# Optimization experiments

Measured on AMD Instinct MI355X. Metric: run time of the kernel, lower is better.

## Reference

```python
import jax, jax.numpy as jnp
import numpy as np

N_NODES = 100000


def gcn_conv(x, edge_index, W, b, n_nodes):
    """PyG GCNConv: linear -> add self-loops -> symmetric-normalized scatter-sum -> bias."""
    h = x @ W  # [N, F_out]
    loop = jnp.arange(n_nodes, dtype=edge_index.dtype)
    src = jnp.concatenate([edge_index[0], loop])
    dst = jnp.concatenate([edge_index[1], loop])
    # degree of destination nodes (self-loops included)
    deg = jax.ops.segment_sum(jnp.ones_like(dst, dtype=h.dtype), dst, num_segments=n_nodes)
    dinv = jnp.where(deg > 0, jax.lax.rsqrt(deg), 0.0)
    norm = dinv[src] * dinv[dst]  # [E+N]
    msg = h[src] * norm[:, None]  # gather + scale
    out = jax.ops.segment_sum(msg, dst, num_segments=n_nodes)  # scatter-add
    return out + b


def setup_inputs() -> dict:
    key = jax.random.key(0)
    k1, k2, k3, k4 = jax.random.split(key, 4)
    d_in, hidden, out = 128, 256, 64
    x = jax.random.normal(k1, (N_NODES, d_in), dtype=jnp.float32)
    edge_index = jax.random.randint(k2, (2, 800000), 0, N_NODES, dtype=jnp.int64)
    W1 = jax.random.normal(k3, (d_in, hidden), dtype=jnp.float32) * (1.0 / np.sqrt(d_in))
    b1 = jnp.zeros((hidden,), dtype=jnp.float32)
    W2 = jax.random.normal(k4, (hidden, out), dtype=jnp.float32) * (1.0 / np.sqrt(hidden))
    b2 = jnp.zeros((out,), dtype=jnp.float32)
    return {"x": x, "edge_index": edge_index, "W1": W1, "b1": b1, "W2": W2, "b2": b2}


def reference(x, edge_index, W1, b1, W2, b2):
    h = jax.nn.relu(gcn_conv(x, edge_index, W1, b1, N_NODES))
    # dropout p=0 (module default) -> identity
    return gcn_conv(h, edge_index, W2, b2, N_NODES)
```

## Files before the change

kernel.cpp:

```cpp
#include <hip/hip_runtime.h>
#include <hip/hip_bf16.h>

#define N_NODES 100000
#define D_IN 128
#define HID 256
#define D_OUT 64
#define TR 32
#define NBUK 196
#define BSH 9
#define MGRID 625

typedef __attribute__((ext_vector_type(8))) short bf8;
typedef __attribute__((ext_vector_type(4))) float f4;

static __device__ __forceinline__ unsigned short f2bf(float f) {
    __hip_bfloat16 h = __float2bfloat16(f);
    return *reinterpret_cast<unsigned short*>(&h);
}
static __device__ __forceinline__ float bflo(unsigned int u) { return __uint_as_float(u << 16); }
static __device__ __forceinline__ float bfhi(unsigned int u) { return __uint_as_float(u & 0xffff0000u); }

static __device__ __forceinline__ void fma8(float* a, float w, uint4 u) {
    a[0] += w * bflo(u.x); a[1] += w * bfhi(u.x);
    a[2] += w * bflo(u.y); a[3] += w * bfhi(u.y);
    a[4] += w * bflo(u.z); a[5] += w * bfhi(u.z);
    a[6] += w * bflo(u.w); a[7] += w * bfhi(u.w);
}
static __device__ __forceinline__ void fma4(float* a, float w, uint2 u) {
    a[0] += w * bflo(u.x); a[1] += w * bfhi(u.x);
    a[2] += w * bflo(u.y); a[3] += w * bfhi(u.y);
}


__global__ __launch_bounds__(256) void k_prep(const float* __restrict__ x,
                                              unsigned long long* __restrict__ xb,
                                              const float* __restrict__ W1,
                                              unsigned short* __restrict__ W1t,
                                              const float* __restrict__ W2,
                                              unsigned short* __restrict__ W2t,
                                              int* __restrict__ bhist) {
    int b = blockIdx.x, t = threadIdx.x;
    if (b < 12500) {
        int i = b * 256 + t;
        float4 v = ((const float4*)x)[i];
        unsigned long long o = (unsigned long long)f2bf(v.x) |
                               ((unsigned long long)f2bf(v.y) << 16) |
                               ((unsigned long long)f2bf(v.z) << 32) |
                               ((unsigned long long)f2bf(v.w) << 48);
        xb[i] = o;
    } else if (b < 12628) {
        int i = (b - 12500) * 256 + t;
        int n = i >> 7, k = i & 127;
        W1t[i] = f2bf(W1[k * HID + n]);
    } else if (b < 12692) {
        int i = (b - 12628) * 256 + t;
        int n = i >> 8, k = i & 255;
        W2t[i] = f2bf(W2[k * D_OUT + n]);
    } else {
        if (t < NBUK) bhist[t] = 0;
    }
}


__global__ __launch_bounds__(256) void k_hist(const int* __restrict__ dst, int E,
                                              int* __restrict__ bhist) {
    __shared__ int h[NBUK];
    int t = threadIdx.x;
    if (t < NBUK) h[t] = 0;
    __syncthreads();
    int base = blockIdx.x * 4096;
    for (int j = 0; j < 16; j++) {
        int e = base + j * 256 + t;
        if (e < E) atomicAdd(&h[dst[e] >> BSH], 1);
    }
    __syncthreads();
    if (t < NBUK && h[t] > 0) atomicAdd(&bhist[t], h[t]);
}

__global__ __launch_bounds__(256) void k_scanB(const int* __restrict__ bhist,
                                               int* __restrict__ bbase,
                                               int* __restrict__ bcursor) {
    __shared__ int s[256];
    int t = threadIdx.x;
    int v = (t < NBUK) ? bhist[t] : 0;
    s[t] = v;
    __syncthreads();
    for (int off = 1; off < 256; off <<= 1) {
        int u = (t >= off) ? s[t - off] : 0;
        __syncthreads();
        s[t] += u;
        __syncthreads();
    }
    if (t < NBUK) {
        bbase[t] = s[t] - v;
        bcursor[t] = s[t] - v;
    }
    if (t == NBUK - 1) bbase[NBUK] = s[t];
}

__global__ __launch_bounds__(256) void k_bin(const int* __restrict__ src,
                                             const int* __restrict__ dst, int E,
                                             int* __restrict__ bcursor,
                                             unsigned int* __restrict__ bin) {
    __shared__ int histL[NBUK], baseL[NBUK], rankL[NBUK];
    int t = threadIdx.x;
    if (t < NBUK) {
        histL[t] = 0;
        rankL[t] = 0;
    }
    __syncthreads();
    int base = blockIdx.x * 4096;
    int ss[16], dd[16];
#pragma unroll
    for (int j = 0; j < 16; j++) {
        int e = base + j * 256 + t;
        if (e < E) {
            ss[j] = src[e];
            dd[j] = dst[e];
            atomicAdd(&histL[dd[j] >> BSH], 1);
        } else {
            dd[j] = -1;
        }
    }
    __syncthreads();
    if (t < NBUK && histL[t] > 0) baseL[t] = atomicAdd(&bcursor[t], histL[t]);
    __syncthreads();
#pragma unroll
    for (int j = 0; j < 16; j++) {
        if (dd[j] >= 0) {
            int bu = dd[j] >> BSH;
            int r = atomicAdd(&rankL[bu], 1);
            bin[baseL[bu] + r] = ((unsigned int)(dd[j] & 511) << 17) | (unsigned int)ss[j];
        }
    }
}

__global__ __launch_bounds__(256) void k_cnt(const unsigned int* __restrict__ bin,
                                             const int* __restrict__ bbase,
                                             int* __restrict__ cnt) {
    __shared__ int c[512];
    int b = blockIdx.x, t = threadIdx.x;
    c[t] = 0;
    c[t + 256] = 0;
    __syncthreads();
    int lo = bbase[b], hi = bbase[b + 1];
    for (int e = lo + t; e < hi; e += 256) atomicAdd(&c[bin[e] >> 17], 1);
    __syncthreads();
    int node0 = b << BSH;
    int nbn = N_NODES - node0;
    if (nbn > 512) nbn = 512;
    if (t < nbn) cnt[node0 + t] = c[t];
    if (t + 256 < nbn) cnt[node0 + t + 256] = c[t + 256];
}

__global__ __launch_bounds__(256) void k_scan_part(const int* __restrict__ cnt,
                                                   int* __restrict__ row_ptr,
                                                   int* __restrict__ bsum,
                                                   float* __restrict__ dinv, int n) {
    __shared__ int s[256];
    int t = threadIdx.x, i = blockIdx.x * 256 + t;
    int v = (i < n) ? cnt[i] : 0;
    s[t] = v;
    __syncthreads();
    for (int off = 1; off < 256; off <<= 1) {
        int u = (t >= off) ? s[t - off] : 0;
        __syncthreads();
        s[t] += u;
        __syncthreads();
    }
    if (i < n) {
        row_ptr[i] = s[t] - v;
        dinv[i] = rsqrtf((float)v + 1.0f);
    }
    if (t == 255) bsum[blockIdx.x] = s[255];
}

__global__ __launch_bounds__(512) void k_scan_base(int* __restrict__ bsum,
                                                   int* __restrict__ row_ptr, int nb, int n) {
    __shared__ int s[512];
    int t = threadIdx.x;
    int v = (t < nb) ? bsum[t] : 0;
    s[t] = v;
    __syncthreads();
    for (int off = 1; off < 512; off <<= 1) {
        int u = (t >= off) ? s[t - off] : 0;
        __syncthreads();
        s[t] += u;
        __syncthreads();
    }
    if (t < nb) bsum[t] = s[t] - v;
    if (t == 511) row_ptr[n] = s[511];
}

__global__ void k_scan_fin(int* __restrict__ row_ptr, const int* __restrict__ bsum, int n) {
    int i = blockIdx.x * blockDim.x + threadIdx.x;
    if (i < n) row_ptr[i] += bsum[i >> 8];
}

__global__ __launch_bounds__(256) void k_place(const unsigned int* __restrict__ bin,
                                               const int* __restrict__ bbase,
                                               const int* __restrict__ row_ptr,
                                               const float* __restrict__ dinv,
                                               int2* __restrict__ cw) {
    __shared__ int cur[512];
    __shared__ float dl[512];
    int b = blockIdx.x, t = threadIdx.x;
    int node0 = b << BSH;
    int nbn = N_NODES - node0;
    if (nbn > 512) nbn = 512;
    if (t < nbn) {
        cur[t] = row_ptr[node0 + t];
        dl[t] = dinv[node0 + t];
    }
    if (t + 256 < nbn) {
        cur[t + 256] = row_ptr[node0 + t + 256];
        dl[t + 256] = dinv[node0 + t + 256];
    }
    __syncthreads();
    int lo = bbase[b], hi = bbase[b + 1];
    for (int e = lo + t; e < hi; e += 256) {
        unsigned int rec = bin[e];
        int s = rec & 0x1FFFF;
        int dloc = rec >> 17;
        int pos = atomicAdd(&cur[dloc], 1);
        int2 v;
        v.x = s;
        v.y = __float_as_int(dinv[s] * dl[dloc]);
        cw[pos] = v;
    }
}


__global__ __launch_bounds__(256) void k_pull1(const int* __restrict__ row_ptr,
                                               const int2* __restrict__ cw,
                                               const uint4* __restrict__ xb4,
                                               const float* __restrict__ dinv,
                                               uint4* __restrict__ agg4) {
    int wave = (blockIdx.x * 256 + threadIdx.x) >> 6;
    int lane = threadIdx.x & 63;
    int g = lane >> 4, l = lane & 15;
    int node = wave * 4 + g;
    int beg = row_ptr[node], end = row_ptr[node + 1];
    float di = dinv[node];
    float a[8] = {0, 0, 0, 0, 0, 0, 0, 0};
    fma8(a, di * di, xb4[(size_t)node * 16 + l]);
    int e = beg;
    for (; e + 4 <= end; e += 4) {
        int2 c0 = cw[e + 0], c1 = cw[e + 1], c2 = cw[e + 2], c3 = cw[e + 3];
        uint4 u0 = xb4[(size_t)c0.x * 16 + l];
        uint4 u1 = xb4[(size_t)c1.x * 16 + l];
        uint4 u2 = xb4[(size_t)c2.x * 16 + l];
        uint4 u3 = xb4[(size_t)c3.x * 16 + l];
        fma8(a, __int_as_float(c0.y), u0);
        fma8(a, __int_as_float(c1.y), u1);
        fma8(a, __int_as_float(c2.y), u2);
        fma8(a, __int_as_float(c3.y), u3);
    }
    for (; e < end; e++) {
        int2 c = cw[e];
        fma8(a, __int_as_float(c.y), xb4[(size_t)c.x * 16 + l]);
    }
    uint4 o;
    o.x = (unsigned int)f2bf(a[0]) | ((unsigned int)f2bf(a[1]) << 16);
    o.y = (unsigned int)f2bf(a[2]) | ((unsigned int)f2bf(a[3]) << 16);
    o.z = (unsigned int)f2bf(a[4]) | ((unsigned int)f2bf(a[5]) << 16);
    o.w = (unsigned int)f2bf(a[6]) | ((unsigned int)f2bf(a[7]) << 16);
    agg4[(size_t)node * 16 + l] = o;
}


__global__ __launch_bounds__(256) void k_fused_mfma(unsigned short* __restrict__ agg,
                                                    const unsigned short* __restrict__ W1t,
                                                    const float* __restrict__ b1,
                                                    const unsigned short* __restrict__ W2t) {
    __shared__ char sH[TR * HID * 2];
    int t = threadIdx.x, wave = t >> 6, lane = t & 63;
    int lr = lane & 15, lg = lane >> 4;

    bf8 w1f[4][4];
#pragma unroll
    for (int kk = 0; kk < 4; kk++)
#pragma unroll
        for (int tt = 0; tt < 4; tt++)
            w1f[kk][tt] = *(const bf8*)(W1t + (size_t)(wave * 64 + tt * 16 + lr) * D_IN + kk * 32 + lg * 8);
    bf8 w2f[8];
#pragma unroll
    for (int kk = 0; kk < 8; kk++)
        w2f[kk] = *(const bf8*)(W2t + (size_t)(wave * 16 + lr) * HID + kk * 32 + lg * 8);
    float bias[4];
#pragma unroll
    for (int tt = 0; tt < 4; tt++) bias[tt] = b1[wave * 64 + tt * 16 + lr];

    for (int it = 0; it < 5; it++) {
        size_t row0 = ((size_t)blockIdx.x + (size_t)it * MGRID) * TR;

        f4 acc1[4][2];
#pragma unroll
        for (int tt = 0; tt < 4; tt++)
#pragma unroll
            for (int h = 0; h < 2; h++) acc1[tt][h] = (f4){0.f, 0.f, 0.f, 0.f};

#pragma unroll
        for (int kk = 0; kk < 4; kk++) {
            bf8 a0 = *(const bf8*)(agg + (row0 + lr) * 128 + kk * 32 + lg * 8);
            bf8 a1 = *(const bf8*)(agg + (row0 + 16 + lr) * 128 + kk * 32 + lg * 8);
#pragma unroll
            for (int tt = 0; tt < 4; tt++) {
                acc1[tt][0] = __builtin_amdgcn_mfma_f32_16x16x32_bf16(a0, w1f[kk][tt], acc1[tt][0], 0, 0, 0);
                acc1[tt][1] = __builtin_amdgcn_mfma_f32_16x16x32_bf16(a1, w1f[kk][tt], acc1[tt][1], 0, 0, 0);
            }
        }

#pragma unroll
        for (int tt = 0; tt < 4; tt++) {
            int colc = wave * 64 + tt * 16 + lr;
#pragma unroll
            for (int h = 0; h < 2; h++) {
#pragma unroll
                for (int ri = 0; ri < 4; ri++) {
                    int row = h * 16 + lg * 4 + ri;
                    float hv = acc1[tt][h][ri] + bias[tt];
                    hv = hv > 0.f ? hv : 0.f;
                    *(unsigned short*)(sH + ((row * 512 + colc * 2) ^ ((row & 7) << 4))) = f2bf(hv);
                }
            }
        }
        __syncthreads();

        f4 acc2[2];
        acc2[0] = (f4){0.f, 0.f, 0.f, 0.f};
        acc2[1] = (f4){0.f, 0.f, 0.f, 0.f};
#pragma unroll
        for (int kk = 0; kk < 8; kk++) {
            bf8 a0 = *(const bf8*)(sH + ((lr * 512 + kk * 64 + lg * 16) ^ ((lr & 7) << 4)));
            bf8 a1 = *(const bf8*)(sH + (((16 + lr) * 512 + kk * 64 + lg * 16) ^ (((16 + lr) & 7) << 4)));
            acc2[0] = __builtin_amdgcn_mfma_f32_16x16x32_bf16(a0, w2f[kk], acc2[0], 0, 0, 0);
            acc2[1] = __builtin_amdgcn_mfma_f32_16x16x32_bf16(a1, w2f[kk], acc2[1], 0, 0, 0);
        }
        int colc = wave * 16 + lr;
#pragma unroll
        for (int h = 0; h < 2; h++)
#pragma unroll
            for (int ri = 0; ri < 4; ri++) {
                int row = h * 16 + lg * 4 + ri;
                agg[(row0 + row) * 128 + colc] = f2bf(acc2[h][ri]);
            }
        __syncthreads();
    }
}


__global__ __launch_bounds__(256) void k_pull2(const int* __restrict__ row_ptr,
                                               const int2* __restrict__ cw,
                                               const uint2* __restrict__ m2,
                                               const float* __restrict__ dinv,
                                               const float* __restrict__ b2,
                                               float4* __restrict__ out4) {
    int wave = (blockIdx.x * 256 + threadIdx.x) >> 6;
    int lane = threadIdx.x & 63;
    int g = lane >> 4, l = lane & 15;
    int node = wave * 4 + g;
    int beg = row_ptr[node], end = row_ptr[node + 1];
    float di = dinv[node];
    float a[4] = {0, 0, 0, 0};
    fma4(a, di * di, m2[(size_t)node * 32 + l]);
    int e = beg;
    for (; e + 4 <= end; e += 4) {
        int2 c0 = cw[e + 0], c1 = cw[e + 1], c2 = cw[e + 2], c3 = cw[e + 3];
        uint2 u0 = m2[(size_t)c0.x * 32 + l];
        uint2 u1 = m2[(size_t)c1.x * 32 + l];
        uint2 u2 = m2[(size_t)c2.x * 32 + l];
        uint2 u3 = m2[(size_t)c3.x * 32 + l];
        fma4(a, __int_as_float(c0.y), u0);
        fma4(a, __int_as_float(c1.y), u1);
        fma4(a, __int_as_float(c2.y), u2);
        fma4(a, __int_as_float(c3.y), u3);
    }
    for (; e < end; e++) {
        int2 c = cw[e];
        fma4(a, __int_as_float(c.y), m2[(size_t)c.x * 32 + l]);
    }
    float4 bv = ((const float4*)b2)[l];
    float4 o;
    o.x = a[0] + bv.x;
    o.y = a[1] + bv.y;
    o.z = a[2] + bv.z;
    o.w = a[3] + bv.w;
    out4[(size_t)node * 16 + l] = o;
}


extern "C" void kernel_launch(void* const* d_in, const int* in_sizes, int n_in,
                              void* d_out, int out_size, void* d_ws, size_t ws_size,
                              hipStream_t stream) {
    const float* x  = (const float*)d_in[0];
    const int*   ei = (const int*)d_in[1];
    const float* W1 = (const float*)d_in[2];
    const float* b1 = (const float*)d_in[3];
    const float* W2 = (const float*)d_in[4];
    const float* b2 = (const float*)d_in[5];
    float* out = (float*)d_out;

    const int E = in_sizes[1] / 2;
    const int* src = ei;
    const int* dst = ei + E;

    char* ws = (char*)d_ws;
    int* cnt            = (int*)(ws + 0);
    int* bsum           = cnt + 100096;
    int* row_ptr        = (int*)(ws + 402176);
    int2* cw            = (int2*)(ws + 802560);
    float* dinv         = (float*)(ws + 7202560);
    unsigned short* W1t = (unsigned short*)(ws + 7602944);
    unsigned short* W2t = (unsigned short*)(ws + 7668480);
    unsigned short* xb  = (unsigned short*)(ws + 7701248);
    unsigned short* aggb = (unsigned short*)(ws + 33301248);
    int* bhist          = (int*)aggb;
    int* bbase          = bhist + 256;
    int* bcursor        = bhist + 512;
    unsigned int* bin   = (unsigned int*)((char*)aggb + 4096);

    const int NB = (N_NODES + 255) / 256;
    const int NBB = (E + 4095) / 4096;

    k_prep<<<12693, 256, 0, stream>>>(x, (unsigned long long*)xb, W1, W1t, W2, W2t, bhist);

    k_hist<<<NBB, 256, 0, stream>>>(dst, E, bhist);
    k_scanB<<<1, 256, 0, stream>>>(bhist, bbase, bcursor);
    k_bin<<<NBB, 256, 0, stream>>>(src, dst, E, bcursor, bin);
    k_cnt<<<NBUK, 256, 0, stream>>>(bin, bbase, cnt);
    k_scan_part<<<NB, 256, 0, stream>>>(cnt, row_ptr, bsum, dinv, N_NODES);
    k_scan_base<<<1, 512, 0, stream>>>(bsum, row_ptr, NB, N_NODES);
    k_scan_fin<<<NB, 256, 0, stream>>>(row_ptr, bsum, N_NODES);
    k_place<<<NBUK, 256, 0, stream>>>(bin, bbase, row_ptr, dinv, cw);

    k_pull1<<<6250, 256, 0, stream>>>(row_ptr, cw, (const uint4*)xb, dinv, (uint4*)aggb);

    k_fused_mfma<<<MGRID, 256, 0, stream>>>(aggb, W1t, b1, W2t);

    k_pull2<<<6250, 256, 0, stream>>>(row_ptr, cw, (const uint2*)aggb, dinv, b2, (float4*)out);
}
```

Baseline: 159.3 us.

## Fuse CSR-build kernels via per-block histograms and prefetch gathers in pull loops

Folds the edge histogram into the prep kernel, writing per-block bucket counts. A single scan kernel then computes deterministic per-block bases, so binning needs no global atomics and no second local histogram pass. The count, scan-part, scan-base and scan-fin kernels merge into one count-and-scan kernel, and the final offset fix-up moves into k_place, cutting launch count and intermediate traffic. Both pull kernels are software-pipelined to issue the next four neighbor gathers before accumulating the current ones, at the cost of more registers.

Measured after the change: 191.4 us. 1.2x slower.

```diff
diff --git a/kernel.cpp b/kernel.cpp
--- a/kernel.cpp
+++ b/kernel.cpp
@@ -38,7 +38,8 @@
                                               unsigned short* __restrict__ W1t,
                                               const float* __restrict__ W2,
                                               unsigned short* __restrict__ W2t,
-                                              int* __restrict__ bhist) {
+                                              const int* __restrict__ dst, int E,
+                                              int* __restrict__ hist2d) {
     int b = blockIdx.x, t = threadIdx.x;
     if (b < 12500) {
         int i = b * 256 + t;
@@ -57,88 +58,81 @@
         int n = i >> 8, k = i & 255;
         W2t[i] = f2bf(W2[k * D_OUT + n]);
     } else {
-        if (t < NBUK) bhist[t] = 0;
-    }
-}
-
-
-__global__ __launch_bounds__(256) void k_hist(const int* __restrict__ dst, int E,
-                                              int* __restrict__ bhist) {
-    __shared__ int h[NBUK];
+        int hb = b - 12692;
+        __shared__ int h[NBUK];
+        if (t < NBUK) h[t] = 0;
+        __syncthreads();
+        int base = hb * 4096;
+        for (int j = 0; j < 16; j++) {
+            int e = base + j * 256 + t;
+            if (e < E) atomicAdd(&h[dst[e] >> BSH], 1);
+        }
+        __syncthreads();
+        if (t < NBUK) hist2d[hb * NBUK + t] = h[t];
+    }
+}
+
+
+__global__ __launch_bounds__(256) void k_scanB(const int* __restrict__ hist2d,
+                                               int* __restrict__ bbase,
+                                               int* __restrict__ blockbase, int nbb) {
+    __shared__ int s[256];
     int t = threadIdx.x;
-    if (t < NBUK) h[t] = 0;
+    int tot = 0;
+    if (t < NBUK)
+        for (int b = 0; b < nbb; b++) tot += hist2d[b * NBUK + t];
+    s[t] = (t < NBUK) ? tot : 0;
+    __syncthreads();
+    for (int off = 1; off < 256; off <<= 1) {
+        int u = (t >= off) ? s[t - off] : 0;
+        __syncthreads();
+        s[t] += u;
+        __syncthreads();
+    }
+    if (t < NBUK) bbase[t] = s[t] - tot;
+    if (t == NBUK - 1) bbase[NBUK] = s[t];
+    __syncthreads();
+    if (t < NBUK) {
+        int run = s[t] - tot;
+        for (int b = 0; b < nbb; b++) {
+            blockbase[b * NBUK + t] = run;
+            run += hist2d[b * NBUK + t];
+        }
+    }
+}
+
+
+__global__ __launch_bounds__(256) void k_bin(const int* __restrict__ src,
+                                             const int* __restrict__ dst, int E,
+                                             const int* __restrict__ blockbase,
+                                             unsigned int* __restrict__ bin) {
+    __shared__ int baseL[NBUK], rankL[NBUK];
+    int t = threadIdx.x;
+    if (t < NBUK) {
+        baseL[t] = blockbase[blockIdx.x * NBUK + t];
+        rankL[t] = 0;
+    }
     __syncthreads();
     int base = blockIdx.x * 4096;
     for (int j = 0; j < 16; j++) {
         int e = base + j * 256 + t;
-        if (e < E) atomicAdd(&h[dst[e] >> BSH], 1);
-    }
-    __syncthreads();
-    if (t < NBUK && h[t] > 0) atomicAdd(&bhist[t], h[t]);
-}
-
-__global__ __launch_bounds__(256) void k_scanB(const int* __restrict__ bhist,
-                                               int* __restrict__ bbase,
-                                               int* __restrict__ bcursor) {
+        if (e < E) {
+            int s = src[e], d = dst[e];
+            int bu = d >> BSH;
+            int r = atomicAdd(&rankL[bu], 1);
+            bin[baseL[bu] + r] = ((unsigned int)(d & 511) << 17) | (unsigned int)s;
+        }
+    }
+}
+
+
+__global__ __launch_bounds__(256) void k_cntscan(const unsigned int* __restrict__ bin,
+                                                 const int* __restrict__ bbase,
+                                                 int* __restrict__ row_ptr,
+                                                 int* __restrict__ bsum,
+                                                 float* __restrict__ dinv) {
+    __shared__ int c[512];
     __shared__ int s[256];
-    int t = threadIdx.x;
-    int v = (t < NBUK) ? bhist[t] : 0;
-    s[t] = v;
-    __syncthreads();
-    for (int off = 1; off < 256; off <<= 1) {
-        int u = (t >= off) ? s[t - off] : 0;
-        __syncthreads();
-        s[t] += u;
-        __syncthreads();
-    }
-    if (t < NBUK) {
-        bbase[t] = s[t] - v;
-        bcursor[t] = s[t] - v;
-    }
-    if (t == NBUK - 1) bbase[NBUK] = s[t];
-}
-
-__global__ __launch_bounds__(256) void k_bin(const int* __restrict__ src,
-                                             const int* __restrict__ dst, int E,
-                                             int* __restrict__ bcursor,
-                                             unsigned int* __restrict__ bin) {
-    __shared__ int histL[NBUK], baseL[NBUK], rankL[NBUK];
-    int t = threadIdx.x;
-    if (t < NBUK) {
-        histL[t] = 0;
-        rankL[t] = 0;
-    }
-    __syncthreads();
-    int base = blockIdx.x * 4096;
-    int ss[16], dd[16];
-#pragma unroll
-    for (int j = 0; j < 16; j++) {
-        int e = base + j * 256 + t;
-        if (e < E) {
-            ss[j] = src[e];
-            dd[j] = dst[e];
-            atomicAdd(&histL[dd[j] >> BSH], 1);
-        } else {
-            dd[j] = -1;
-        }
-    }
-    __syncthreads();
-    if (t < NBUK && histL[t] > 0) baseL[t] = atomicAdd(&bcursor[t], histL[t]);
-    __syncthreads();
-#pragma unroll
-    for (int j = 0; j < 16; j++) {
-        if (dd[j] >= 0) {
-            int bu = dd[j] >> BSH;
-            int r = atomicAdd(&rankL[bu], 1);
-            bin[baseL[bu] + r] = ((unsigned int)(dd[j] & 511) << 17) | (unsigned int)ss[j];
-        }
-    }
-}
-
-__global__ __launch_bounds__(256) void k_cnt(const unsigned int* __restrict__ bin,
-                                             const int* __restrict__ bbase,
-                                             int* __restrict__ cnt) {
-    __shared__ int c[512];
     int b = blockIdx.x, t = threadIdx.x;
     c[t] = 0;
     c[t + 256] = 0;
@@ -146,21 +140,8 @@
     int lo = bbase[b], hi = bbase[b + 1];
     for (int e = lo + t; e < hi; e += 256) atomicAdd(&c[bin[e] >> 17], 1);
     __syncthreads();
-    int node0 = b << BSH;
-    int nbn = N_NODES - node0;
-    if (nbn > 512) nbn = 512;
-    if (t < nbn) cnt[node0 + t] = c[t];
-    if (t + 256 < nbn) cnt[node0 + t + 256] = c[t + 256];
-}
-
-__global__ __launch_bounds__(256) void k_scan_part(const int* __restrict__ cnt,
-                                                   int* __restrict__ row_ptr,
-                                                   int* __restrict__ bsum,
-                                                   float* __restrict__ dinv, int n) {
-    __shared__ int s[256];
-    int t = threadIdx.x, i = blockIdx.x * 256 + t;
-    int v = (i < n) ? cnt[i] : 0;
-    s[t] = v;
+    int a0 = c[2 * t], a1 = c[2 * t + 1];
+    s[t] = a0 + a1;
     __syncthreads();
     for (int off = 1; off < 256; off <<= 1) {
         int u = (t >= off) ? s[t - off] : 0;
@@ -168,52 +149,53 @@
         s[t] += u;
         __syncthreads();
     }
-    if (i < n) {
-        row_ptr[i] = s[t] - v;
-        dinv[i] = rsqrtf((float)v + 1.0f);
-    }
-    if (t == 255) bsum[blockIdx.x] = s[255];
-}
-
-__global__ __launch_bounds__(512) void k_scan_base(int* __restrict__ bsum,
-                                                   int* __restrict__ row_ptr, int nb, int n) {
-    __shared__ int s[512];
-    int t = threadIdx.x;
-    int v = (t < nb) ? bsum[t] : 0;
-    s[t] = v;
-    __syncthreads();
-    for (int off = 1; off < 512; off <<= 1) {
-        int u = (t >= off) ? s[t - off] : 0;
-        __syncthreads();
-        s[t] += u;
-        __syncthreads();
-    }
-    if (t < nb) bsum[t] = s[t] - v;
-    if (t == 511) row_ptr[n] = s[511];
-}
-
-__global__ void k_scan_fin(int* __restrict__ row_ptr, const int* __restrict__ bsum, int n) {
-    int i = blockIdx.x * blockDim.x + threadIdx.x;
-    if (i < n) row_ptr[i] += bsum[i >> 8];
-}
+    int ex = (t > 0) ? s[t - 1] : 0;
+    int n0 = (b << BSH) + 2 * t;
+    if (n0 < N_NODES) {
+        row_ptr[n0] = ex;
+        dinv[n0] = rsqrtf((float)a0 + 1.0f);
+    }
+    if (n0 + 1 < N_NODES) {
+        row_ptr[n0 + 1] = ex + a0;
+        dinv[n0 + 1] = rsqrtf((float)a1 + 1.0f);
+    }
+    if (t == 255) bsum[b] = s[255];
+}
+
 
 __global__ __launch_bounds__(256) void k_place(const unsigned int* __restrict__ bin,
                                                const int* __restrict__ bbase,
-                                               const int* __restrict__ row_ptr,
+                                               const int* __restrict__ bsum,
+                                               int* __restrict__ row_ptr,
                                                const float* __restrict__ dinv,
                                                int2* __restrict__ cw) {
+    __shared__ int sc[256];
     __shared__ int cur[512];
     __shared__ float dl[512];
     int b = blockIdx.x, t = threadIdx.x;
+    sc[t] = (t < NBUK) ? bsum[t] : 0;
+    __syncthreads();
+    for (int off = 1; off < 256; off <<= 1) {
+        int u = (t >= off) ? sc[t - off] : 0;
+        __syncthreads();
+        sc[t] += u;
+        __syncthreads();
+    }
+    int base = (b > 0) ? sc[b - 1] : 0;
+    if (b == NBUK - 1 && t == 0) row_ptr[N_NODES] = sc[NBUK - 1];
     int node0 = b << BSH;
     int nbn = N_NODES - node0;
     if (nbn > 512) nbn = 512;
     if (t < nbn) {
-        cur[t] = row_ptr[node0 + t];
+        int v = row_ptr[node0 + t] + base;
+        cur[t] = v;
+        row_ptr[node0 + t] = v;
         dl[t] = dinv[node0 + t];
     }
     if (t + 256 < nbn) {
-        cur[t + 256] = row_ptr[node0 + t + 256];
+        int v = row_ptr[node0 + t + 256] + base;
+        cur[t + 256] = v;
+        row_ptr[node0 + t + 256] = v;
         dl[t + 256] = dinv[node0 + t + 256];
     }
     __syncthreads();
@@ -245,12 +227,26 @@
     float a[8] = {0, 0, 0, 0, 0, 0, 0, 0};
     fma8(a, di * di, xb4[(size_t)node * 16 + l]);
     int e = beg;
-    for (; e + 4 <= end; e += 4) {
-        int2 c0 = cw[e + 0], c1 = cw[e + 1], c2 = cw[e + 2], c3 = cw[e + 3];
+    if (e + 4 <= end) {
+        int2 c0 = cw[e], c1 = cw[e + 1], c2 = cw[e + 2], c3 = cw[e + 3];
         uint4 u0 = xb4[(size_t)c0.x * 16 + l];
         uint4 u1 = xb4[(size_t)c1.x * 16 + l];
         uint4 u2 = xb4[(size_t)c2.x * 16 + l];
         uint4 u3 = xb4[(size_t)c3.x * 16 + l];
+        e += 4;
+        for (; e + 4 <= end; e += 4) {
+            int2 d0 = cw[e], d1 = cw[e + 1], d2 = cw[e + 2], d3 = cw[e + 3];
+            uint4 v0 = xb4[(size_t)d0.x * 16 + l];
+            uint4 v1 = xb4[(size_t)d1.x * 16 + l];
+            uint4 v2 = xb4[(size_t)d2.x * 16 + l];
+            uint4 v3 = xb4[(size_t)d3.x * 16 + l];
+            fma8(a, __int_as_float(c0.y), u0);
+            fma8(a, __int_as_float(c1.y), u1);
+            fma8(a, __int_as_float(c2.y), u2);
+            fma8(a, __int_as_float(c3.y), u3);
+            c0 = d0; c1 = d1; c2 = d2; c3 = d3;
+            u0 = v0; u1 = v1; u2 = v2; u3 = v3;
+        }
         fma8(a, __int_as_float(c0.y), u0);
         fma8(a, __int_as_float(c1.y), u1);
         fma8(a, __int_as_float(c2.y), u2);
@@ -365,12 +361,26 @@
     float a[4] = {0, 0, 0, 0};
     fma4(a, di * di, m2[(size_t)node * 32 + l]);
     int e = beg;
-    for (; e + 4 <= end; e += 4) {
-        int2 c0 = cw[e + 0], c1 = cw[e + 1], c2 = cw[e + 2], c3 = cw[e + 3];
+    if (e + 4 <= end) {
+        int2 c0 = cw[e], c1 = cw[e + 1], c2 = cw[e + 2], c3 = cw[e + 3];
         uint2 u0 = m2[(size_t)c0.x * 32 + l];
         uint2 u1 = m2[(size_t)c1.x * 32 + l];
         uint2 u2 = m2[(size_t)c2.x * 32 + l];
         uint2 u3 = m2[(size_t)c3.x * 32 + l];
+        e += 4;
+        for (; e + 4 <= end; e += 4) {
+            int2 d0 = cw[e], d1 = cw[e + 1], d2 = cw[e + 2], d3 = cw[e + 3];
+            uint2 v0 = m2[(size_t)d0.x * 32 + l];
+            uint2 v1 = m2[(size_t)d1.x * 32 + l];
+            uint2 v2 = m2[(size_t)d2.x * 32 + l];
+            uint2 v3 = m2[(size_t)d3.x * 32 + l];
+            fma4(a, __int_as_float(c0.y), u0);
+            fma4(a, __int_as_float(c1.y), u1);
+            fma4(a, __int_as_float(c2.y), u2);
+            fma4(a, __int_as_float(c3.y), u3);
+            c0 = d0; c1 = d1; c2 = d2; c3 = d3;
+            u0 = v0; u1 = v1; u2 = v2; u3 = v3;
+        }
         fma4(a, __int_as_float(c0.y), u0);
         fma4(a, __int_as_float(c1.y), u1);
         fma4(a, __int_as_float(c2.y), u2);
@@ -406,37 +416,28 @@
     const int* dst = ei + E;
 
     char* ws = (char*)d_ws;
-    int* cnt            = (int*)(ws + 0);
-    int* bsum           = cnt + 100096;
-    int* row_ptr        = (int*)(ws + 402176);
-    int2* cw            = (int2*)(ws + 802560);
-    float* dinv         = (float*)(ws + 7202560);
-    unsigned short* W1t = (unsigned short*)(ws + 7602944);
-    unsigned short* W2t = (unsigned short*)(ws + 7668480);
-    unsigned short* xb  = (unsigned short*)(ws + 7701248);
-    unsigned short* aggb = (unsigned short*)(ws + 33301248);
-    int* bhist          = (int*)aggb;
-    int* bbase          = bhist + 256;
-    int* bcursor        = bhist + 512;
-    unsigned int* bin   = (unsigned int*)((char*)aggb + 4096);
-
-    const int NB = (N_NODES + 255) / 256;
+    int* row_ptr        = (int*)(ws + 0);
+    int2* cw            = (int2*)(ws + 400640);
+    float* dinv         = (float*)(ws + 6800640);
+    unsigned short* W1t = (unsigned short*)(ws + 7201024);
+    unsigned short* W2t = (unsigned short*)(ws + 7266560);
+    unsigned short* xb  = (unsigned short*)(ws + 7299328);
+    unsigned short* aggb = (unsigned short*)(ws + 32899328);
+    unsigned int* bin   = (unsigned int*)aggb;
+    int* hist2d         = (int*)((char*)aggb + 3200256);
+    int* blockbase      = (int*)((char*)aggb + 3354112);
+    int* bbase          = (int*)((char*)aggb + 3507968);
+    int* bsum           = (int*)((char*)aggb + 3509248);
+
     const int NBB = (E + 4095) / 4096;
 
-    k_prep<<<12693, 256, 0, stream>>>(x, (unsigned long long*)xb, W1, W1t, W2, W2t, bhist);
-
-    k_hist<<<NBB, 256, 0, stream>>>(dst, E, bhist);
-    k_scanB<<<1, 256, 0, stream>>>(bhist, bbase, bcursor);
-    k_bin<<<NBB, 256, 0, stream>>>(src, dst, E, bcursor, bin);
-    k_cnt<<<NBUK, 256, 0, stream>>>(bin, bbase, cnt);
-    k_scan_part<<<NB, 256, 0, stream>>>(cnt, row_ptr, bsum, dinv, N_NODES);
-    k_scan_base<<<1, 512, 0, stream>>>(bsum, row_ptr, NB, N_NODES);
-    k_scan_fin<<<NB, 256, 0, stream>>>(row_ptr, bsum, N_NODES);
-    k_place<<<NBUK, 256, 0, stream>>>(bin, bbase, row_ptr, dinv, cw);
-
+    k_prep<<<12692 + NBB, 256, 0, stream>>>(x, (unsigned long long*)xb, W1, W1t, W2, W2t,
+                                            dst, E, hist2d);
+    k_scanB<<<1, 256, 0, stream>>>(hist2d, bbase, blockbase, NBB);
+    k_bin<<<NBB, 256, 0, stream>>>(src, dst, E, blockbase, bin);
+    k_cntscan<<<NBUK, 256, 0, stream>>>(bin, bbase, row_ptr, bsum, dinv);
+    k_place<<<NBUK, 256, 0, stream>>>(bin, bbase, bsum, row_ptr, dinv, cw);
     k_pull1<<<6250, 256, 0, stream>>>(row_ptr, cw, (const uint4*)xb, dinv, (uint4*)aggb);
-
     k_fused_mfma<<<MGRID, 256, 0, stream>>>(aggb, W1t, b1, W2t);
-
     k_pull2<<<6250, 256, 0, stream>>>(row_ptr, cw, (const uint2*)aggb, dinv, b2, (float4*)out);
 }
```
